# Performance work log

Hardware: AMD Instinct MI355X
Metric: run time of the kernel (lower is better)

The kernel has to match this reference:

```python
import jax, jax.numpy as jnp
import numpy as np

H = 8          # num_heads
D = 64         # out_dims = input_dims / num_heads
DM = H * D     # input_dims = 512
B, S = 2, 2048


def _linear(x, W, b):
    # torch nn.Linear: x @ W.T + b, W: [out, in]
    return jnp.einsum('...d,ed->...e', x, W) + b


def setup_inputs() -> dict:
    key = jax.random.key(0)
    ks = jax.random.split(key, 12)
    inp = {
        'query': jax.random.normal(ks[0], (B, S, DM), dtype=jnp.float32),
        'key': jax.random.normal(ks[1], (B, S, DM), dtype=jnp.float32),
        'value': jax.random.normal(ks[2], (B, S, DM), dtype=jnp.float32),
        'Wq': jax.random.normal(ks[3], (D, D), dtype=jnp.float32) * 0.02,
        'bq': jnp.zeros((D,), dtype=jnp.float32),
        'Wk': jax.random.normal(ks[4], (D, D), dtype=jnp.float32) * 0.02,
        'bk': jnp.zeros((D,), dtype=jnp.float32),
        'Wv': jax.random.normal(ks[5], (D, D), dtype=jnp.float32) * 0.02,
        'bv': jnp.zeros((D,), dtype=jnp.float32),
        'Wo': jax.random.normal(ks[6], (DM, DM), dtype=jnp.float32) * 0.02,
        'bo': jnp.zeros((DM,), dtype=jnp.float32),
        'mask': jax.random.randint(ks[7], (B, 1, 1, S), 0, 2, dtype=jnp.int32),
    }
    return inp


def reference(query, key, value, Wq, bq, Wk, bk, Wv, bv, Wo, bo, mask):
    b, qlen = query.shape[0], query.shape[1]
    klen = key.shape[1]
    # split heads: [B, S, H, D]
    q = _linear(query.reshape(b, qlen, H, D), Wq, bq)
    k = _linear(key.reshape(b, klen, H, D), Wk, bk)
    v = _linear(value.reshape(b, klen, H, D), Wv, bv)
    # scores: [B, H, Q, K]
    attn = jnp.einsum('bqhd,bkhd->bhqk', q, k)
    attn = jnp.where(mask == 0, jnp.float32(-1e20), attn)
    # NOTE: original scale is num_heads ** 1 / 2 == H / 2 (Python precedence quirk)
    score = jax.nn.softmax(attn * (2.0 / H), axis=-1)
    # out einsum gives [B, Q, D, H]; flattening gives (d, h) feature order
    out = jnp.einsum('bhqv,bvhd->bqdh', score, v)
    out = out.reshape(b, qlen, D * H)
    return _linear(out, Wo, bo)
```

## Files before the change

### kernel.cpp

```cpp
#include <hip/hip_runtime.h>
#include <math.h>

typedef float f32x4 __attribute__((ext_vector_type(4)));
typedef short s16x8 __attribute__((ext_vector_type(8)));
typedef unsigned short ushort_t;

namespace {
constexpr int kH  = 8;
constexpr int kD  = 64;
constexpr int kDM = 512;
constexpr int kB  = 2;
constexpr int kS  = 2048;
constexpr size_t kNE = (size_t)kB * kS * kDM;
constexpr size_t kNL = (size_t)kB * kH * kS;
}

__device__ __forceinline__ void split_bf16(float x, ushort_t& hi, ushort_t& lo) {
  union { float f; unsigned u; } a; a.f = x;
  hi = (ushort_t)(a.u >> 16);
  union { unsigned u; float f; } hh; hh.u = a.u & 0xffff0000u;
  union { float f; unsigned u; } r; r.f = x - hh.f;
  lo = (ushort_t)(r.u >> 16);
}
__device__ __forceinline__ ushort_t rne_bf16(float x) {
  union { float f; unsigned u; } a; a.f = x;
  const unsigned t = a.u + 0x7fffu + ((a.u >> 16) & 1u);
  return (ushort_t)(t >> 16);
}

__global__ __launch_bounds__(256)
void w_split_kernel(const float* __restrict__ Wo, const float* __restrict__ Wq,
                    const float* __restrict__ Wk, const float* __restrict__ Wv,
                    ushort_t* __restrict__ wo_h, ushort_t* __restrict__ wo_l,
                    ushort_t* __restrict__ wq_h, ushort_t* __restrict__ wq_l,
                    ushort_t* __restrict__ wk_h, ushort_t* __restrict__ wk_l,
                    ushort_t* __restrict__ wv_h, ushort_t* __restrict__ wv_l) {
  const int bid = blockIdx.x;
  if (bid < 256) {
    const int i = (bid * 256 + threadIdx.x) * 4;
    const float4 v = *(const float4*)&Wo[i];
    const int e = i >> 9;
    const float vv[4] = {v.x, v.y, v.z, v.w};
    #pragma unroll
    for (int j = 0; j < 4; ++j) {
      const int f = (i & 511) + j;
      const int g = (f & 7) * 64 + (f >> 3);
      ushort_t hi, lo;
      split_bf16(vv[j], hi, lo);
      wo_h[(size_t)e * kDM + g] = hi;
      wo_l[(size_t)e * kDM + g] = lo;
    }
  } else {
    const int which = bid - 256;
    const float* W = (which == 0) ? Wq : (which == 1) ? Wk : Wv;
    ushort_t* oh = (which == 0) ? wq_h : (which == 1) ? wk_h : wv_h;
    ushort_t* ol = (which == 0) ? wq_l : (which == 1) ? wk_l : wv_l;
    #pragma unroll
    for (int cc = 0; cc < 4; ++cc) {
      const int i = (cc * 256 + threadIdx.x) * 4;
      const float4 v = *(const float4*)&W[i];
      ushort_t h[4], l[4];
      split_bf16(v.x, h[0], l[0]);
      split_bf16(v.y, h[1], l[1]);
      split_bf16(v.z, h[2], l[2]);
      split_bf16(v.w, h[3], l[3]);
      int2 hp, lp;
      hp.x = (int)((unsigned)h[0] | ((unsigned)h[1] << 16));
      hp.y = (int)((unsigned)h[2] | ((unsigned)h[3] << 16));
      lp.x = (int)((unsigned)l[0] | ((unsigned)l[1] << 16));
      lp.y = (int)((unsigned)l[2] | ((unsigned)l[3] << 16));
      *(int2*)&oh[i] = hp;
      *(int2*)&ol[i] = lp;
    }
  }
}

__global__ __launch_bounds__(256, 2)
void kv_proj_kernel(const float* __restrict__ xk, const float* __restrict__ xv,
                    const ushort_t* __restrict__ wk_h, const ushort_t* __restrict__ wk_l,
                    const float* __restrict__ bk,
                    const ushort_t* __restrict__ wv_h, const ushort_t* __restrict__ wv_l,
                    const float* __restrict__ bv,
                    ushort_t* __restrict__ k_hi, ushort_t* __restrict__ vt_hi) {
  __shared__ __align__(16) ushort_t Xh[64][72];
  __shared__ __align__(16) ushort_t Xl[64][72];
  const int which = blockIdx.z;
  const float* x = which ? xv : xk;
  const ushort_t* wh = which ? wv_h : wk_h;
  const ushort_t* wl = which ? wv_l : wk_l;
  const float* bias = which ? bv : bk;
  const int h = blockIdx.y;
  const int t0g = blockIdx.x * 64;
  const int b = t0g >> 11, s0 = t0g & (kS - 1);
  const int tid  = threadIdx.x;
  const int w    = tid >> 6;
  const int lane = tid & 63;
  const int ln   = lane & 15;
  const int quad = lane >> 4;
  const size_t hb = ((size_t)b * kH + h) * (size_t)(kS * kD);

  #pragma unroll
  for (int cc = 0; cc < 4; ++cc) {
    const int id = tid + cc * 256;
    const int r = id >> 4, c = id & 15;
    const float4 v = *(const float4*)&x[((size_t)t0g + r) * kDM + h * kD + c * 4];
    ushort_t hh[4], ll[4];
    split_bf16(v.x, hh[0], ll[0]);
    split_bf16(v.y, hh[1], ll[1]);
    split_bf16(v.z, hh[2], ll[2]);
    split_bf16(v.w, hh[3], ll[3]);
    int2 hp, lp;
    hp.x = (int)((unsigned)hh[0] | ((unsigned)hh[1] << 16));
    hp.y = (int)((unsigned)hh[2] | ((unsigned)hh[3] << 16));
    lp.x = (int)((unsigned)ll[0] | ((unsigned)ll[1] << 16));
    lp.y = (int)((unsigned)ll[2] | ((unsigned)ll[3] << 16));
    *(int2*)&Xh[r][c * 4] = hp;
    *(int2*)&Xl[r][c * 4] = lp;
  }
  __syncthreads();

  f32x4 C[4];
  #pragma unroll
  for (int eb = 0; eb < 4; ++eb) C[eb] = (f32x4){0.f, 0.f, 0.f, 0.f};
  #pragma unroll
  for (int kc = 0; kc < 2; ++kc) {
    const s16x8 ah = *(const s16x8*)&Xh[w * 16 + ln][kc * 32 + quad * 8];
    const s16x8 al = *(const s16x8*)&Xl[w * 16 + ln][kc * 32 + quad * 8];
    s16x8 bh[4], bl[4];
    #pragma unroll
    for (int eb = 0; eb < 4; ++eb) {
      bh[eb] = *(const s16x8*)&wh[(size_t)(eb * 16 + ln) * kD + kc * 32 + quad * 8];
      bl[eb] = *(const s16x8*)&wl[(size_t)(eb * 16 + ln) * kD + kc * 32 + quad * 8];
    }
    #pragma unroll
    for (int eb = 0; eb < 4; ++eb)
      C[eb] = __builtin_amdgcn_mfma_f32_16x16x32_bf16(ah, bh[eb], C[eb], 0, 0, 0);
    #pragma unroll
    for (int eb = 0; eb < 4; ++eb)
      C[eb] = __builtin_amdgcn_mfma_f32_16x16x32_bf16(ah, bl[eb], C[eb], 0, 0, 0);
    #pragma unroll
    for (int eb = 0; eb < 4; ++eb)
      C[eb] = __builtin_amdgcn_mfma_f32_16x16x32_bf16(al, bh[eb], C[eb], 0, 0, 0);
  }
  __syncthreads();

  if (which == 0) {
    #pragma unroll
    for (int eb = 0; eb < 4; ++eb) {
      const float be = bias[eb * 16 + ln];
      #pragma unroll
      for (int r = 0; r < 4; ++r)
        Xh[w * 16 + quad * 4 + r][eb * 16 + ln] = rne_bf16(C[eb][r] + be);
    }
    __syncthreads();
    #pragma unroll
    for (int cc = 0; cc < 2; ++cc) {
      const int id = tid + cc * 256;
      const int r = id >> 3, c = id & 7;
      *(int4*)&k_hi[hb + (size_t)(s0 + r) * kD + c * 8] = *(int4*)&Xh[r][c * 8];
    }
  } else {
    #pragma unroll
    for (int eb = 0; eb < 4; ++eb) {
      const float be = bias[eb * 16 + ln];
      #pragma unroll
      for (int r = 0; r < 4; ++r)
        Xh[eb * 16 + ln][w * 16 + quad * 4 + r] = rne_bf16(C[eb][r] + be);
    }
    __syncthreads();
    #pragma unroll
    for (int cc = 0; cc < 2; ++cc) {
      const int id = tid + cc * 256;
      const int r = id >> 3, c = id & 7;
      *(int4*)&vt_hi[hb + (size_t)r * kS + s0 + c * 8] = *(int4*)&Xh[r][c * 8];
    }
  }
}

__global__ __launch_bounds__(512, 6)
void attn_kernel(const float* __restrict__ xq,
                 const ushort_t* __restrict__ wq_h, const ushort_t* __restrict__ wq_l,
                 const float* __restrict__ bq,
                 const ushort_t* __restrict__ k_hi, const ushort_t* __restrict__ vt_hi,
                 const int* __restrict__ mask,
                 float* __restrict__ O32, float* __restrict__ lws) {
  __shared__ __align__(16) unsigned char smem[34816];
  __shared__ float Mz[64];
  ushort_t (*Kh)[72] = (ushort_t(*)[72])smem;
  ushort_t (*Vh)[72] = (ushort_t(*)[72])(smem + 9216);
  ushort_t (*Pb)[16][40] = (ushort_t(*)[16][40])(smem + 18432);
  unsigned (*QT)[68] = (unsigned(*)[68])smem;

  const int tid  = threadIdx.x;
  const int w    = tid >> 6;
  const int lane = tid & 63;
  const int ln   = lane & 15;
  const int quad = lane >> 4;
  const int h    = blockIdx.y;
  const int b    = blockIdx.z >> 2;
  const int quarter = blockIdx.z & 3;
  const int q0   = blockIdx.x * 128;
  const size_t hb = ((size_t)b * kH + h) * (size_t)(kS * kD);

  s16x8 aqh[2], aql[2];
  {
    const int qrow = q0 + w * 16 + ln;
    f32x4 C[4];
    #pragma unroll
    for (int eb = 0; eb < 4; ++eb) C[eb] = (f32x4){0.f, 0.f, 0.f, 0.f};
    #pragma unroll
    for (int kc = 0; kc < 2; ++kc) {
      const float* xp = &xq[((size_t)b * kS + qrow) * kDM + h * kD + kc * 32 + quad * 8];
      const float4 x0 = *(const float4*)xp;
      const float4 x1 = *(const float4*)(xp + 4);
      const float xs[8] = {x0.x, x0.y, x0.z, x0.w, x1.x, x1.y, x1.z, x1.w};
      s16x8 ah, al;
      #pragma unroll
      for (int j = 0; j < 8; ++j) {
        ushort_t hi, lo;
        split_bf16(xs[j], hi, lo);
        ah[j] = (short)hi; al[j] = (short)lo;
      }
      s16x8 bh[4], bl[4];
      #pragma unroll
      for (int eb = 0; eb < 4; ++eb) {
        bh[eb] = *(const s16x8*)&wq_h[(size_t)(eb * 16 + ln) * kD + kc * 32 + quad * 8];
        bl[eb] = *(const s16x8*)&wq_l[(size_t)(eb * 16 + ln) * kD + kc * 32 + quad * 8];
      }
      #pragma unroll
      for (int eb = 0; eb < 4; ++eb)
        C[eb] = __builtin_amdgcn_mfma_f32_16x16x32_bf16(ah, bh[eb], C[eb], 0, 0, 0);
      #pragma unroll
      for (int eb = 0; eb < 4; ++eb)
        C[eb] = __builtin_amdgcn_mfma_f32_16x16x32_bf16(ah, bl[eb], C[eb], 0, 0, 0);
      #pragma unroll
      for (int eb = 0; eb < 4; ++eb)
        C[eb] = __builtin_amdgcn_mfma_f32_16x16x32_bf16(al, bh[eb], C[eb], 0, 0, 0);
    }
    #pragma unroll
    for (int eb = 0; eb < 4; ++eb) {
      const float be = bq[eb * 16 + ln];
      #pragma unroll
      for (int r = 0; r < 4; ++r) {
        ushort_t hi, lo;
        split_bf16(C[eb][r] + be, hi, lo);
        QT[w * 16 + quad * 4 + r][eb * 16 + ln] = ((unsigned)hi << 16) | (unsigned)lo;
      }
    }
    #pragma unroll
    for (int db = 0; db < 2; ++db) {
      const uint4 u0 = *(const uint4*)&QT[w * 16 + ln][db * 32 + quad * 8];
      const uint4 u1 = *(const uint4*)&QT[w * 16 + ln][db * 32 + quad * 8 + 4];
      const unsigned uu[8] = {u0.x, u0.y, u0.z, u0.w, u1.x, u1.y, u1.z, u1.w};
      #pragma unroll
      for (int j = 0; j < 8; ++j) {
        aqh[db][j] = (short)(uu[j] >> 16);
        aql[db][j] = (short)(uu[j] & 0xffffu);
      }
    }
  }
  __syncthreads();

  f32x4 O[4];
  #pragma unroll
  for (int db = 0; db < 4; ++db) O[db] = (f32x4){0.f, 0.f, 0.f, 0.f};
  float rs[4] = {0.f, 0.f, 0.f, 0.f};

  const int kt0 = quarter * 8;
  for (int kt = kt0; kt < kt0 + 8; ++kt) {
    __syncthreads();
    {
      const ushort_t* gkh = k_hi + hb + (size_t)kt * 64 * kD;
      const ushort_t* gvh = vt_hi + hb + (size_t)kt * 64;
      const int r = tid >> 3, c = tid & 7;
      *(int4*)&Kh[r][c * 8] = *(const int4*)&gkh[r * kD + c * 8];
      *(int4*)&Vh[r][c * 8] = *(const int4*)&gvh[(size_t)r * kS + c * 8];
      if (tid < 64) Mz[tid] = (mask[(size_t)b * kS + kt * 64 + tid] != 0) ? 1.0f : 0.0f;
    }
    __syncthreads();

    #pragma unroll
    for (int h32 = 0; h32 < 2; ++h32) {
      f32x4 C[2];
      C[0] = (f32x4){0.f, 0.f, 0.f, 0.f};
      C[1] = (f32x4){0.f, 0.f, 0.f, 0.f};
      #pragma unroll
      for (int db = 0; db < 2; ++db) {
        const s16x8 bh0 = *(const s16x8*)&Kh[h32 * 32 + ln][db * 32 + quad * 8];
        const s16x8 bh1 = *(const s16x8*)&Kh[h32 * 32 + 16 + ln][db * 32 + quad * 8];
        C[0] = __builtin_amdgcn_mfma_f32_16x16x32_bf16(aqh[db], bh0, C[0], 0, 0, 0);
        C[1] = __builtin_amdgcn_mfma_f32_16x16x32_bf16(aqh[db], bh1, C[1], 0, 0, 0);
        C[0] = __builtin_amdgcn_mfma_f32_16x16x32_bf16(aql[db], bh0, C[0], 0, 0, 0);
        C[1] = __builtin_amdgcn_mfma_f32_16x16x32_bf16(aql[db], bh1, C[1], 0, 0, 0);
      }
      #pragma unroll
      for (int kb = 0; kb < 2; ++kb) {
        const float mz = Mz[h32 * 32 + kb * 16 + ln];
        #pragma unroll
        for (int r = 0; r < 4; ++r) {
          const float p = mz * __expf(0.25f * C[kb][r]);
          union { float f; unsigned u; } pa; pa.f = p;
          const unsigned t = pa.u + 0x7fffu + ((pa.u >> 16) & 1u);
          Pb[w][quad * 4 + r][kb * 16 + ln] = (ushort_t)(t >> 16);
          union { unsigned u; float f; } pr; pr.u = t & 0xffff0000u;
          rs[r] += pr.f;
        }
      }
      {
        const s16x8 ph = *(const s16x8*)&Pb[w][ln][quad * 8];
        s16x8 vh[4];
        #pragma unroll
        for (int db = 0; db < 4; ++db)
          vh[db] = *(const s16x8*)&Vh[db * 16 + ln][h32 * 32 + quad * 8];
        #pragma unroll
        for (int db = 0; db < 4; ++db)
          O[db] = __builtin_amdgcn_mfma_f32_16x16x32_bf16(ph, vh[db], O[db], 0, 0, 0);
      }
    }
  }

  #pragma unroll
  for (int m = 1; m < 16; m <<= 1) {
    #pragma unroll
    for (int r = 0; r < 4; ++r) rs[r] += __shfl_xor(rs[r], m);
  }
  if (ln == 0) {
    float* lp = lws + ((size_t)b * kH + h) * kS + q0 + w * 16 + quad * 4;
    #pragma unroll
    for (int r = 0; r < 4; ++r) atomicAdd(&lp[r], rs[r]);
  }
  const size_t obase = ((size_t)b * kS + q0 + w * 16 + quad * 4) * kDM + h * kD;
  #pragma unroll
  for (int db = 0; db < 4; ++db) {
    #pragma unroll
    for (int r = 0; r < 4; ++r)
      atomicAdd(&O32[obase + (size_t)r * kDM + db * 16 + ln], O[db][r]);
  }
}

__global__ __launch_bounds__(256, 2)
void out_proj_kernel(const float* __restrict__ O32, const float* __restrict__ lws,
                     const ushort_t* __restrict__ wh, const ushort_t* __restrict__ wl,
                     const float* __restrict__ bo, float* __restrict__ out) {
  __shared__ __align__(16) ushort_t Ah[64][72];
  __shared__ __align__(16) ushort_t Al[64][72];
  __shared__ __align__(16) ushort_t Bh[64][72];
  __shared__ __align__(16) ushort_t Bl[64][72];
  __shared__ float linv[kH][64];
  const int t0 = blockIdx.x * 64;
  const int e0 = blockIdx.y * 64;
  const int b  = t0 >> 11;
  const int s0 = t0 & (kS - 1);
  const int tid  = threadIdx.x;
  const int w    = tid >> 6;
  const int lane = tid & 63;
  const int ln   = lane & 15;
  const int quad = lane >> 4;

  for (int id = tid; id < kH * 64; id += 256) {
    const int hh = id >> 6, r = id & 63;
    linv[hh][r] = 1.0f / lws[((size_t)b * kH + hh) * kS + s0 + r];
  }

  f32x4 C[4];
  #pragma unroll
  for (int eb = 0; eb < 4; ++eb) C[eb] = (f32x4){0.f, 0.f, 0.f, 0.f};

  for (int k0 = 0; k0 < kDM; k0 += 64) {
    __syncthreads();
    const int hh = k0 >> 6;
    #pragma unroll
    for (int cc = 0; cc < 4; ++cc) {
      const int id = tid + cc * 256;
      const int r = id >> 4, c4 = id & 15;
      float4 v = *(const float4*)&O32[(size_t)(t0 + r) * kDM + k0 + c4 * 4];
      const float li = linv[hh][r];
      v.x *= li; v.y *= li; v.z *= li; v.w *= li;
      ushort_t h4[4], l4[4];
      split_bf16(v.x, h4[0], l4[0]);
      split_bf16(v.y, h4[1], l4[1]);
      split_bf16(v.z, h4[2], l4[2]);
      split_bf16(v.w, h4[3], l4[3]);
      int2 hp, lp;
      hp.x = (int)((unsigned)h4[0] | ((unsigned)h4[1] << 16));
      hp.y = (int)((unsigned)h4[2] | ((unsigned)h4[3] << 16));
      lp.x = (int)((unsigned)l4[0] | ((unsigned)l4[1] << 16));
      lp.y = (int)((unsigned)l4[2] | ((unsigned)l4[3] << 16));
      *(int2*)&Ah[r][c4 * 4] = hp;
      *(int2*)&Al[r][c4 * 4] = lp;
    }
    #pragma unroll
    for (int cc = 0; cc < 2; ++cc) {
      const int id = tid + cc * 256;
      const int r = id >> 3, off = (id & 7) * 8;
      *(int4*)&Bh[r][off] = *(const int4*)&wh[(size_t)(e0 + r) * kDM + k0 + off];
      *(int4*)&Bl[r][off] = *(const int4*)&wl[(size_t)(e0 + r) * kDM + k0 + off];
    }
    __syncthreads();
    #pragma unroll
    for (int kc = 0; kc < 2; ++kc) {
      const s16x8 ah = *(const s16x8*)&Ah[w * 16 + ln][kc * 32 + quad * 8];
      const s16x8 al = *(const s16x8*)&Al[w * 16 + ln][kc * 32 + quad * 8];
      s16x8 bh[4], bl[4];
      #pragma unroll
      for (int eb = 0; eb < 4; ++eb) {
        bh[eb] = *(const s16x8*)&Bh[eb * 16 + ln][kc * 32 + quad * 8];
        bl[eb] = *(const s16x8*)&Bl[eb * 16 + ln][kc * 32 + quad * 8];
      }
      #pragma unroll
      for (int eb = 0; eb < 4; ++eb)
        C[eb] = __builtin_amdgcn_mfma_f32_16x16x32_bf16(ah, bh[eb], C[eb], 0, 0, 0);
      #pragma unroll
      for (int eb = 0; eb < 4; ++eb)
        C[eb] = __builtin_amdgcn_mfma_f32_16x16x32_bf16(ah, bl[eb], C[eb], 0, 0, 0);
      #pragma unroll
      for (int eb = 0; eb < 4; ++eb)
        C[eb] = __builtin_amdgcn_mfma_f32_16x16x32_bf16(al, bh[eb], C[eb], 0, 0, 0);
    }
  }

  #pragma unroll
  for (int eb = 0; eb < 4; ++eb) {
    const int e = e0 + eb * 16 + ln;
    const float be = bo[e];
    #pragma unroll
    for (int r = 0; r < 4; ++r) {
      const int t = t0 + w * 16 + quad * 4 + r;
      out[(size_t)t * kDM + e] = C[eb][r] + be;
    }
  }
}

extern "C" void kernel_launch(void* const* d_in, const int* in_sizes, int n_in,
                              void* d_out, int out_size, void* d_ws, size_t ws_size,
                              hipStream_t stream) {
  const float* query = (const float*)d_in[0];
  const float* key   = (const float*)d_in[1];
  const float* value = (const float*)d_in[2];
  const float* Wq = (const float*)d_in[3];
  const float* bq = (const float*)d_in[4];
  const float* Wk = (const float*)d_in[5];
  const float* bk = (const float*)d_in[6];
  const float* Wv = (const float*)d_in[7];
  const float* bv = (const float*)d_in[8];
  const float* Wo = (const float*)d_in[9];
  const float* bo = (const float*)d_in[10];
  const int* mask = (const int*)d_in[11];
  float* out = (float*)d_out;

  ushort_t* k_hi  = (ushort_t*)d_ws;
  ushort_t* vt_hi = k_hi + kNE;
  ushort_t* wo_h  = vt_hi + kNE;
  ushort_t* wo_l  = wo_h + (size_t)kDM * kDM;
  float*    O32   = (float*)(wo_l + (size_t)kDM * kDM);
  float*    lws   = O32 + kNE;
  ushort_t* wq_h  = (ushort_t*)(lws + kNL);
  ushort_t* wq_l  = wq_h + kD * kD;
  ushort_t* wk_h  = wq_l + kD * kD;
  ushort_t* wk_l  = wk_h + kD * kD;
  ushort_t* wv_h  = wk_l + kD * kD;
  ushort_t* wv_l  = wv_h + kD * kD;

  hipMemsetAsync(O32, 0, (kNE + kNL) * sizeof(float), stream);
  w_split_kernel<<<dim3(259), 256, 0, stream>>>(
      Wo, Wq, Wk, Wv, wo_h, wo_l, wq_h, wq_l, wk_h, wk_l, wv_h, wv_l);
  kv_proj_kernel<<<dim3(kB * kS / 64, kH, 2), 256, 0, stream>>>(
      key, value, wk_h, wk_l, bk, wv_h, wv_l, bv, k_hi, vt_hi);
  attn_kernel<<<dim3(kS / 128, kH, kB * 4), 512, 0, stream>>>(
      query, wq_h, wq_l, bq, k_hi, vt_hi, mask, O32, lws);
  out_proj_kernel<<<dim3(kB * kS / 64, kDM / 64), 256, 0, stream>>>(
      O32, lws, wo_h, wo_l, bo, out);
}
```

Measured before the change: 186.4 us.

## Replace fp32 atomic split-K accumulation with bf16 partial buffers and drop Q low split

The attention kernel no longer atomically adds fp32 partial outputs and row sums into a zeroed buffer. Each key-quarter now writes its bf16 partial O tile through shared memory, plus its row sums, to its own slice, and the output projection sums the four slices. This removes the memset and the atomic traffic. Blocks shrink to 256 threads, each wave handling 32 query rows so K/V fragments are reused twice. The Q low-bf16 correction term is dropped, halving QK MFMAs at some cost in accuracy, and the Wo split kernel is reorganised to write 16-byte vectors.

```diff
diff --git a/kernel.cpp b/kernel.cpp
--- a/kernel.cpp
+++ b/kernel.cpp
@@ -27,6 +27,9 @@
   const unsigned t = a.u + 0x7fffu + ((a.u >> 16) & 1u);
   return (ushort_t)(t >> 16);
 }
+__device__ __forceinline__ float bf_to_f(unsigned u16) {
+  union { unsigned u; float f; } a; a.u = u16 << 16; return a.f;
+}
 
 __global__ __launch_bounds__(256)
 void w_split_kernel(const float* __restrict__ Wo, const float* __restrict__ Wq,
@@ -36,22 +39,28 @@
                     ushort_t* __restrict__ wk_h, ushort_t* __restrict__ wk_l,
                     ushort_t* __restrict__ wv_h, ushort_t* __restrict__ wv_l) {
   const int bid = blockIdx.x;
-  if (bid < 256) {
-    const int i = (bid * 256 + threadIdx.x) * 4;
-    const float4 v = *(const float4*)&Wo[i];
-    const int e = i >> 9;
-    const float vv[4] = {v.x, v.y, v.z, v.w};
-    #pragma unroll
-    for (int j = 0; j < 4; ++j) {
-      const int f = (i & 511) + j;
-      const int g = (f & 7) * 64 + (f >> 3);
-      ushort_t hi, lo;
-      split_bf16(vv[j], hi, lo);
-      wo_h[(size_t)e * kDM + g] = hi;
-      wo_l[(size_t)e * kDM + g] = lo;
-    }
+  if (bid < 128) {
+    const int gi = (bid * 256 + threadIdx.x) * 8;
+    const int e  = gi >> 9;
+    const int g0 = gi & 511;
+    const int fbase = (g0 & 63) * 8 + (g0 >> 6);
+    ushort_t h[8], l[8];
+    #pragma unroll
+    for (int j = 0; j < 8; ++j)
+      split_bf16(Wo[(size_t)e * kDM + fbase + j * 8], h[j], l[j]);
+    int4 hp, lp;
+    hp.x = (int)((unsigned)h[0] | ((unsigned)h[1] << 16));
+    hp.y = (int)((unsigned)h[2] | ((unsigned)h[3] << 16));
+    hp.z = (int)((unsigned)h[4] | ((unsigned)h[5] << 16));
+    hp.w = (int)((unsigned)h[6] | ((unsigned)h[7] << 16));
+    lp.x = (int)((unsigned)l[0] | ((unsigned)l[1] << 16));
+    lp.y = (int)((unsigned)l[2] | ((unsigned)l[3] << 16));
+    lp.z = (int)((unsigned)l[4] | ((unsigned)l[5] << 16));
+    lp.w = (int)((unsigned)l[6] | ((unsigned)l[7] << 16));
+    *(int4*)&wo_h[(size_t)e * kDM + g0] = hp;
+    *(int4*)&wo_l[(size_t)e * kDM + g0] = lp;
   } else {
-    const int which = bid - 256;
+    const int which = bid - 128;
     const float* W = (which == 0) ? Wq : (which == 1) ? Wk : Wv;
     ushort_t* oh = (which == 0) ? wq_h : (which == 1) ? wk_h : wv_h;
     ushort_t* ol = (which == 0) ? wq_l : (which == 1) ? wk_l : wv_l;
@@ -177,19 +186,20 @@
   }
 }
 
-__global__ __launch_bounds__(512, 6)
+__global__ __launch_bounds__(256, 4)
 void attn_kernel(const float* __restrict__ xq,
                  const ushort_t* __restrict__ wq_h, const ushort_t* __restrict__ wq_l,
                  const float* __restrict__ bq,
                  const ushort_t* __restrict__ k_hi, const ushort_t* __restrict__ vt_hi,
                  const int* __restrict__ mask,
-                 float* __restrict__ O32, float* __restrict__ lws) {
-  __shared__ __align__(16) unsigned char smem[34816];
+                 ushort_t* __restrict__ Opart, float* __restrict__ lws) {
+  __shared__ __align__(16) ushort_t smem[128 * 72];
+  __shared__ __align__(16) ushort_t Pbm[4 * 32 * 40];
   __shared__ float Mz[64];
+  ushort_t (*QT)[72] = (ushort_t(*)[72])smem;
   ushort_t (*Kh)[72] = (ushort_t(*)[72])smem;
-  ushort_t (*Vh)[72] = (ushort_t(*)[72])(smem + 9216);
-  ushort_t (*Pb)[16][40] = (ushort_t(*)[16][40])(smem + 18432);
-  unsigned (*QT)[68] = (unsigned(*)[68])smem;
+  ushort_t (*Vh)[72] = (ushort_t(*)[72])(smem + 64 * 72);
+  ushort_t (*Pb)[32][40] = (ushort_t(*)[32][40])Pbm;
 
   const int tid  = threadIdx.x;
   const int w    = tid >> 6;
@@ -202,9 +212,10 @@
   const int q0   = blockIdx.x * 128;
   const size_t hb = ((size_t)b * kH + h) * (size_t)(kS * kD);
 
-  s16x8 aqh[2], aql[2];
-  {
-    const int qrow = q0 + w * 16 + ln;
+  s16x8 aqh[2][2];
+  #pragma unroll
+  for (int g = 0; g < 2; ++g) {
+    const int qrow = q0 + w * 32 + g * 16 + ln;
     f32x4 C[4];
     #pragma unroll
     for (int eb = 0; eb < 4; ++eb) C[eb] = (f32x4){0.f, 0.f, 0.f, 0.f};
@@ -221,50 +232,34 @@
         split_bf16(xs[j], hi, lo);
         ah[j] = (short)hi; al[j] = (short)lo;
       }
-      s16x8 bh[4], bl[4];
       #pragma unroll
       for (int eb = 0; eb < 4; ++eb) {
-        bh[eb] = *(const s16x8*)&wq_h[(size_t)(eb * 16 + ln) * kD + kc * 32 + quad * 8];
-        bl[eb] = *(const s16x8*)&wq_l[(size_t)(eb * 16 + ln) * kD + kc * 32 + quad * 8];
-      }
-      #pragma unroll
-      for (int eb = 0; eb < 4; ++eb)
-        C[eb] = __builtin_amdgcn_mfma_f32_16x16x32_bf16(ah, bh[eb], C[eb], 0, 0, 0);
-      #pragma unroll
-      for (int eb = 0; eb < 4; ++eb)
-        C[eb] = __builtin_amdgcn_mfma_f32_16x16x32_bf16(ah, bl[eb], C[eb], 0, 0, 0);
-      #pragma unroll
-      for (int eb = 0; eb < 4; ++eb)
-        C[eb] = __builtin_amdgcn_mfma_f32_16x16x32_bf16(al, bh[eb], C[eb], 0, 0, 0);
+        const s16x8 bh = *(const s16x8*)&wq_h[(size_t)(eb * 16 + ln) * kD + kc * 32 + quad * 8];
+        const s16x8 bl = *(const s16x8*)&wq_l[(size_t)(eb * 16 + ln) * kD + kc * 32 + quad * 8];
+        C[eb] = __builtin_amdgcn_mfma_f32_16x16x32_bf16(ah, bh, C[eb], 0, 0, 0);
+        C[eb] = __builtin_amdgcn_mfma_f32_16x16x32_bf16(ah, bl, C[eb], 0, 0, 0);
+        C[eb] = __builtin_amdgcn_mfma_f32_16x16x32_bf16(al, bh, C[eb], 0, 0, 0);
+      }
     }
     #pragma unroll
     for (int eb = 0; eb < 4; ++eb) {
       const float be = bq[eb * 16 + ln];
       #pragma unroll
-      for (int r = 0; r < 4; ++r) {
-        ushort_t hi, lo;
-        split_bf16(C[eb][r] + be, hi, lo);
-        QT[w * 16 + quad * 4 + r][eb * 16 + ln] = ((unsigned)hi << 16) | (unsigned)lo;
-      }
-    }
-    #pragma unroll
-    for (int db = 0; db < 2; ++db) {
-      const uint4 u0 = *(const uint4*)&QT[w * 16 + ln][db * 32 + quad * 8];
-      const uint4 u1 = *(const uint4*)&QT[w * 16 + ln][db * 32 + quad * 8 + 4];
-      const unsigned uu[8] = {u0.x, u0.y, u0.z, u0.w, u1.x, u1.y, u1.z, u1.w};
-      #pragma unroll
-      for (int j = 0; j < 8; ++j) {
-        aqh[db][j] = (short)(uu[j] >> 16);
-        aql[db][j] = (short)(uu[j] & 0xffffu);
-      }
-    }
+      for (int r = 0; r < 4; ++r)
+        QT[w * 32 + g * 16 + quad * 4 + r][eb * 16 + ln] = rne_bf16(C[eb][r] + be);
+    }
+    #pragma unroll
+    for (int db = 0; db < 2; ++db)
+      aqh[g][db] = *(const s16x8*)&QT[w * 32 + g * 16 + ln][db * 32 + quad * 8];
   }
   __syncthreads();
 
-  f32x4 O[4];
-  #pragma unroll
-  for (int db = 0; db < 4; ++db) O[db] = (f32x4){0.f, 0.f, 0.f, 0.f};
-  float rs[4] = {0.f, 0.f, 0.f, 0.f};
+  f32x4 O[2][4];
+  #pragma unroll
+  for (int g = 0; g < 2; ++g)
+    #pragma unroll
+    for (int db = 0; db < 4; ++db) O[g][db] = (f32x4){0.f, 0.f, 0.f, 0.f};
+  float rs[2][4] = {};
 
   const int kt0 = quarter * 8;
   for (int kt = kt0; kt < kt0 + 8; ++kt) {
@@ -272,49 +267,60 @@
     {
       const ushort_t* gkh = k_hi + hb + (size_t)kt * 64 * kD;
       const ushort_t* gvh = vt_hi + hb + (size_t)kt * 64;
-      const int r = tid >> 3, c = tid & 7;
-      *(int4*)&Kh[r][c * 8] = *(const int4*)&gkh[r * kD + c * 8];
-      *(int4*)&Vh[r][c * 8] = *(const int4*)&gvh[(size_t)r * kS + c * 8];
+      #pragma unroll
+      for (int cc = 0; cc < 2; ++cc) {
+        const int id = tid + cc * 256;
+        const int r = id >> 3, c = id & 7;
+        *(int4*)&Kh[r][c * 8] = *(const int4*)&gkh[r * kD + c * 8];
+        *(int4*)&Vh[r][c * 8] = *(const int4*)&gvh[(size_t)r * kS + c * 8];
+      }
       if (tid < 64) Mz[tid] = (mask[(size_t)b * kS + kt * 64 + tid] != 0) ? 1.0f : 0.0f;
     }
     __syncthreads();
 
     #pragma unroll
     for (int h32 = 0; h32 < 2; ++h32) {
-      f32x4 C[2];
-      C[0] = (f32x4){0.f, 0.f, 0.f, 0.f};
-      C[1] = (f32x4){0.f, 0.f, 0.f, 0.f};
+      f32x4 C[2][2];
+      #pragma unroll
+      for (int g = 0; g < 2; ++g) {
+        C[g][0] = (f32x4){0.f, 0.f, 0.f, 0.f};
+        C[g][1] = (f32x4){0.f, 0.f, 0.f, 0.f};
+      }
       #pragma unroll
       for (int db = 0; db < 2; ++db) {
         const s16x8 bh0 = *(const s16x8*)&Kh[h32 * 32 + ln][db * 32 + quad * 8];
         const s16x8 bh1 = *(const s16x8*)&Kh[h32 * 32 + 16 + ln][db * 32 + quad * 8];
-        C[0] = __builtin_amdgcn_mfma_f32_16x16x32_bf16(aqh[db], bh0, C[0], 0, 0, 0);
-        C[1] = __builtin_amdgcn_mfma_f32_16x16x32_bf16(aqh[db], bh1, C[1], 0, 0, 0);
-        C[0] = __builtin_amdgcn_mfma_f32_16x16x32_bf16(aql[db], bh0, C[0], 0, 0, 0);
-        C[1] = __builtin_amdgcn_mfma_f32_16x16x32_bf16(aql[db], bh1, C[1], 0, 0, 0);
-      }
-      #pragma unroll
-      for (int kb = 0; kb < 2; ++kb) {
-        const float mz = Mz[h32 * 32 + kb * 16 + ln];
         #pragma unroll
-        for (int r = 0; r < 4; ++r) {
-          const float p = mz * __expf(0.25f * C[kb][r]);
-          union { float f; unsigned u; } pa; pa.f = p;
-          const unsigned t = pa.u + 0x7fffu + ((pa.u >> 16) & 1u);
-          Pb[w][quad * 4 + r][kb * 16 + ln] = (ushort_t)(t >> 16);
-          union { unsigned u; float f; } pr; pr.u = t & 0xffff0000u;
-          rs[r] += pr.f;
+        for (int g = 0; g < 2; ++g) {
+          C[g][0] = __builtin_amdgcn_mfma_f32_16x16x32_bf16(aqh[g][db], bh0, C[g][0], 0, 0, 0);
+          C[g][1] = __builtin_amdgcn_mfma_f32_16x16x32_bf16(aqh[g][db], bh1, C[g][1], 0, 0, 0);
         }
       }
+      #pragma unroll
+      for (int g = 0; g < 2; ++g) {
+        #pragma unroll
+        for (int kb = 0; kb < 2; ++kb) {
+          const float mz = Mz[h32 * 32 + kb * 16 + ln];
+          #pragma unroll
+          for (int r = 0; r < 4; ++r) {
+            const float p = mz * __expf(0.25f * C[g][kb][r]);
+            union { float f; unsigned u; } pa; pa.f = p;
+            const unsigned t = pa.u + 0x7fffu + ((pa.u >> 16) & 1u);
+            Pb[w][g * 16 + quad * 4 + r][kb * 16 + ln] = (ushort_t)(t >> 16);
+            union { unsigned u; float f; } pr; pr.u = t & 0xffff0000u;
+            rs[g][r] += pr.f;
+          }
+        }
+      }
       {
-        const s16x8 ph = *(const s16x8*)&Pb[w][ln][quad * 8];
-        s16x8 vh[4];
+        const s16x8 ph0 = *(const s16x8*)&Pb[w][ln][quad * 8];
+        const s16x8 ph1 = *(const s16x8*)&Pb[w][16 + ln][quad * 8];
         #pragma unroll
-        for (int db = 0; db < 4; ++db)
-          vh[db] = *(const s16x8*)&Vh[db * 16 + ln][h32 * 32 + quad * 8];
-        #pragma unroll
-        for (int db = 0; db < 4; ++db)
-          O[db] = __builtin_amdgcn_mfma_f32_16x16x32_bf16(ph, vh[db], O[db], 0, 0, 0);
+        for (int db = 0; db < 4; ++db) {
+          const s16x8 vh = *(const s16x8*)&Vh[db * 16 + ln][h32 * 32 + quad * 8];
+          O[0][db] = __builtin_amdgcn_mfma_f32_16x16x32_bf16(ph0, vh, O[0][db], 0, 0, 0);
+          O[1][db] = __builtin_amdgcn_mfma_f32_16x16x32_bf16(ph1, vh, O[1][db], 0, 0, 0);
+        }
       }
     }
   }
@@ -322,24 +328,40 @@
   #pragma unroll
   for (int m = 1; m < 16; m <<= 1) {
     #pragma unroll
-    for (int r = 0; r < 4; ++r) rs[r] += __shfl_xor(rs[r], m);
+    for (int g = 0; g < 2; ++g)
+      #pragma unroll
+      for (int r = 0; r < 4; ++r) rs[g][r] += __shfl_xor(rs[g][r], m);
   }
   if (ln == 0) {
-    float* lp = lws + ((size_t)b * kH + h) * kS + q0 + w * 16 + quad * 4;
-    #pragma unroll
-    for (int r = 0; r < 4; ++r) atomicAdd(&lp[r], rs[r]);
-  }
-  const size_t obase = ((size_t)b * kS + q0 + w * 16 + quad * 4) * kDM + h * kD;
-  #pragma unroll
-  for (int db = 0; db < 4; ++db) {
-    #pragma unroll
-    for (int r = 0; r < 4; ++r)
-      atomicAdd(&O32[obase + (size_t)r * kDM + db * 16 + ln], O[db][r]);
+    #pragma unroll
+    for (int g = 0; g < 2; ++g) {
+      float* lp = lws + (size_t)quarter * kNL + ((size_t)b * kH + h) * kS +
+                  q0 + w * 32 + g * 16 + quad * 4;
+      #pragma unroll
+      for (int r = 0; r < 4; ++r) lp[r] = rs[g][r];
+    }
+  }
+
+  __syncthreads();
+  #pragma unroll
+  for (int g = 0; g < 2; ++g)
+    #pragma unroll
+    for (int db = 0; db < 4; ++db)
+      #pragma unroll
+      for (int r = 0; r < 4; ++r)
+        QT[w * 32 + g * 16 + quad * 4 + r][db * 16 + ln] = rne_bf16(O[g][db][r]);
+  __syncthreads();
+  ushort_t* op = Opart + (size_t)quarter * kNE;
+  #pragma unroll
+  for (int cc = 0; cc < 4; ++cc) {
+    const int id = tid + cc * 256;
+    const int r = id >> 3, c = id & 7;
+    *(int4*)&op[((size_t)b * kS + q0 + r) * kDM + h * kD + c * 8] = *(int4*)&QT[r][c * 8];
   }
 }
 
 __global__ __launch_bounds__(256, 2)
-void out_proj_kernel(const float* __restrict__ O32, const float* __restrict__ lws,
+void out_proj_kernel(const ushort_t* __restrict__ Opart, const float* __restrict__ lws,
                      const ushort_t* __restrict__ wh, const ushort_t* __restrict__ wl,
                      const float* __restrict__ bo, float* __restrict__ out) {
   __shared__ __align__(16) ushort_t Ah[64][72];
@@ -359,7 +381,9 @@
 
   for (int id = tid; id < kH * 64; id += 256) {
     const int hh = id >> 6, r = id & 63;
-    linv[hh][r] = 1.0f / lws[((size_t)b * kH + hh) * kS + s0 + r];
+    const size_t base = ((size_t)b * kH + hh) * kS + s0 + r;
+    linv[hh][r] = 1.0f / (lws[base] + lws[kNL + base] +
+                          lws[2 * kNL + base] + lws[3 * kNL + base]);
   }
 
   f32x4 C[4];
@@ -373,14 +397,23 @@
     for (int cc = 0; cc < 4; ++cc) {
       const int id = tid + cc * 256;
       const int r = id >> 4, c4 = id & 15;
-      float4 v = *(const float4*)&O32[(size_t)(t0 + r) * kDM + k0 + c4 * 4];
+      const size_t off = (size_t)(t0 + r) * kDM + k0 + c4 * 4;
+      float a0 = 0.f, a1 = 0.f, a2 = 0.f, a3 = 0.f;
+      #pragma unroll
+      for (int q = 0; q < 4; ++q) {
+        const int2 u = *(const int2*)&Opart[(size_t)q * kNE + off];
+        a0 += bf_to_f((unsigned)u.x & 0xffffu);
+        a1 += bf_to_f((unsigned)u.x >> 16);
+        a2 += bf_to_f((unsigned)u.y & 0xffffu);
+        a3 += bf_to_f((unsigned)u.y >> 16);
+      }
       const float li = linv[hh][r];
-      v.x *= li; v.y *= li; v.z *= li; v.w *= li;
+      a0 *= li; a1 *= li; a2 *= li; a3 *= li;
       ushort_t h4[4], l4[4];
-      split_bf16(v.x, h4[0], l4[0]);
-      split_bf16(v.y, h4[1], l4[1]);
-      split_bf16(v.z, h4[2], l4[2]);
-      split_bf16(v.w, h4[3], l4[3]);
+      split_bf16(a0, h4[0], l4[0]);
+      split_bf16(a1, h4[1], l4[1]);
+      split_bf16(a2, h4[2], l4[2]);
+      split_bf16(a3, h4[3], l4[3]);
       int2 hp, lp;
       hp.x = (int)((unsigned)h4[0] | ((unsigned)h4[1] << 16));
       hp.y = (int)((unsigned)h4[2] | ((unsigned)h4[3] << 16));
@@ -452,22 +485,21 @@
   ushort_t* vt_hi = k_hi + kNE;
   ushort_t* wo_h  = vt_hi + kNE;
   ushort_t* wo_l  = wo_h + (size_t)kDM * kDM;
-  float*    O32   = (float*)(wo_l + (size_t)kDM * kDM);
-  float*    lws   = O32 + kNE;
-  ushort_t* wq_h  = (ushort_t*)(lws + kNL);
+  ushort_t* Opart = wo_l + (size_t)kDM * kDM;
+  float*    lws   = (float*)(Opart + 4 * kNE);
+  ushort_t* wq_h  = (ushort_t*)(lws + 4 * kNL);
   ushort_t* wq_l  = wq_h + kD * kD;
   ushort_t* wk_h  = wq_l + kD * kD;
   ushort_t* wk_l  = wk_h + kD * kD;
   ushort_t* wv_h  = wk_l + kD * kD;
   ushort_t* wv_l  = wv_h + kD * kD;
 
-  hipMemsetAsync(O32, 0, (kNE + kNL) * sizeof(float), stream);
-  w_split_kernel<<<dim3(259), 256, 0, stream>>>(
+  w_split_kernel<<<dim3(131), 256, 0, stream>>>(
       Wo, Wq, Wk, Wv, wo_h, wo_l, wq_h, wq_l, wk_h, wk_l, wv_h, wv_l);
   kv_proj_kernel<<<dim3(kB * kS / 64, kH, 2), 256, 0, stream>>>(
       key, value, wk_h, wk_l, bk, wv_h, wv_l, bv, k_hi, vt_hi);
-  attn_kernel<<<dim3(kS / 128, kH, kB * 4), 512, 0, stream>>>(
-      query, wq_h, wq_l, bq, k_hi, vt_hi, mask, O32, lws);
+  attn_kernel<<<dim3(kS / 128, kH, kB * 4), 256, 0, stream>>>(
+      query, wq_h, wq_l, bq, k_hi, vt_hi, mask, Opart, lws);
   out_proj_kernel<<<dim3(kB * kS / 64, kDM / 64), 256, 0, stream>>>(
-      O32, lws, wo_h, wo_l, bo, out);
-}
+      Opart, lws, wo_h, wo_l, bo, out);
+}
```

Result: faster. 173.6 us (-6.9%).
